# Kernel tuning notes

Measured on AMD Instinct MI355X. Metric: run time of the kernel, lower is better.

The kernel has to match this reference:

```python
import jax, jax.numpy as jnp
import numpy as np

N_NODES = 50000


def _gcn_conv(x, row, col, W, b, n_nodes):
    # symmetric-norm GCN conv with self loops already appended to (row, col)
    deg = jax.ops.segment_sum(jnp.ones_like(row, dtype=x.dtype), row, num_segments=n_nodes)
    # every node has a self loop, so deg >= 1; pow(-0.5) is finite
    dis = deg ** -0.5
    norm = dis[row] * dis[col]                       # [E']
    msg = x[row] * norm[:, None]                     # gather + scale  [E', d]
    agg = jax.ops.segment_sum(msg, col, num_segments=n_nodes)  # scatter-add [N, d]
    return agg @ W + b


def setup_inputs() -> dict:
    key = jax.random.key(0)
    ks = jax.random.split(key, 12)
    N, E, Q, d_in, h = N_NODES, 800000, 200000, 64, 128
    x = jax.random.normal(ks[0], (N, d_in), dtype=jnp.float32)
    edge_index = jax.random.randint(ks[1], (2, E), 0, N)
    edge_label_index = jax.random.randint(ks[2], (2, Q), 0, N)
    def lin(k, fan_in, fan_out):
        kw, kb = jax.random.split(k)
        bound = 1.0 / np.sqrt(fan_in)
        W = jax.random.uniform(kw, (fan_in, fan_out), minval=-bound, maxval=bound, dtype=jnp.float32)
        b = jax.random.uniform(kb, (fan_out,), minval=-bound, maxval=bound, dtype=jnp.float32)
        return W, b
    W1, b1 = lin(ks[3], d_in, h)
    W2, b2 = lin(ks[4], h, h)
    Wc1, bc1 = lin(ks[5], 2 * h, h)
    Wc2, bc2 = lin(ks[6], h, 1)
    return {"x": x, "edge_index": edge_index, "edge_label_index": edge_label_index,
            "W1": W1, "b1": b1, "W2": W2, "b2": b2,
            "Wc1": Wc1, "bc1": bc1, "Wc2": Wc2, "bc2": bc2}


def reference(x, edge_index, edge_label_index, W1, b1, W2, b2, Wc1, bc1, Wc2, bc2):
    n = x.shape[0]
    loops = jnp.arange(n, dtype=edge_index.dtype)
    row = jnp.concatenate([edge_index[0], loops])
    col = jnp.concatenate([edge_index[1], loops])
    h1 = jax.nn.relu(_gcn_conv(x, row, col, W1, b1, n))
    h2 = _gcn_conv(h1, row, col, W2, b2, n)
    src, dst = edge_label_index[0], edge_label_index[1]
    h = jnp.concatenate([h2[src], h2[dst]], axis=1)  # [Q, 2*hidden]
    h = jax.nn.relu(h @ Wc1 + bc1)
    return h @ Wc2 + bc2                              # [Q, 1]
```

## Files before the change

kernel.cpp:

```cpp
#include <hip/hip_runtime.h>


#define HB 64
#define NWIN 16384

typedef __attribute__((ext_vector_type(8))) short short8;
typedef __attribute__((ext_vector_type(4))) float floatx4;

static __device__ __forceinline__ unsigned int f2bf(float v) {
    union { float f; unsigned int u; } c; c.f = v;
    unsigned int lsb = (c.u >> 16) & 1u;
    c.u += 0x7FFFu + lsb;
    return c.u >> 16;
}
static __device__ __forceinline__ float bf2f(unsigned int h) {
    union { float f; unsigned int u; } c; c.u = h << 16;
    return c.f;
}

__global__ __launch_bounds__(256) void k_pre(const int* __restrict__ row,
                                             const int* __restrict__ col,
                                             unsigned int* __restrict__ hRow,
                                             unsigned int* __restrict__ hCol,
                                             const float* __restrict__ x,
                                             unsigned int* __restrict__ xb,
                                             const float* __restrict__ W1,
                                             const float* __restrict__ W2,
                                             const float* __restrict__ Wc1,
                                             const float* __restrict__ b2,
                                             const float* __restrict__ bc1,
                                             unsigned short* __restrict__ UVhi,
                                             unsigned short* __restrict__ UVlo,
                                             unsigned short* __restrict__ W1hi,
                                             unsigned short* __restrict__ W1lo,
                                             float* __restrict__ buv,
                                             int E, int N, int W, int chunk,
                                             int nHist, int nXb) {
    __shared__ unsigned int lds[NWIN];
    int t = threadIdx.x, b = blockIdx.x;
    if (b < nHist) {
        int hb = b % HB;
        int yb = b / HB;
        int p = yb >> 1, win = yb & 1;
        int base = win * NWIN;
        int wcap = min(W - base, NWIN);
        if (wcap <= 0) return;
        const int* idxArr = p ? col : row;
        unsigned int* outArr = p ? hCol : hRow;
        int e0 = hb * chunk, e1 = min(E, e0 + chunk);
        for (int i = t; i < wcap; i += 256) lds[i] = 0;
        __syncthreads();
        for (int e = e0 + t; e < e1; e += 256) {
            int idx = idxArr[e];
            int w = (idx >> 1) - base;
            if ((unsigned)w < (unsigned)wcap)
                atomicAdd(&lds[w], 1u << ((idx & 1) * 16));
        }
        __syncthreads();
        for (int i = t; i < wcap; i += 256)
            outArr[(size_t)hb * W + base + i] = lds[i];
    } else if (b < nHist + nXb) {
        int i = (b - nHist) * 256 + t;
        if (i < N * 32) {
            float2 v = ((const float2*)x)[i];
            xb[i] = f2bf(v.x) | (f2bf(v.y) << 16);
        }
    } else {
        int bf = b - nHist - nXb;
        float* w2row = (float*)lds;
        if (bf < 128) {
            int k = bf;
            int j = t & 127, half = t >> 7;
            int n = half * 128 + j;
            const float* wc = Wc1 + (size_t)half * 128 * 128 + j;
            if (t < 128) w2row[t] = W2[k * 128 + t];
            __syncthreads();
            float acc = 0.f;
#pragma unroll 8
            for (int m = 0; m < 128; m++) acc += w2row[m] * wc[(size_t)m * 128];
            int kstep = k >> 5, kl = k & 31, quad = kl >> 3, j8 = kl & 7;
            int nb = n >> 4, l = quad * 16 + (n & 15);
            int pidx = ((kstep * 16 + nb) * 64 + l) * 8 + j8;
            unsigned int h = f2bf(acc);
            UVhi[pidx] = (unsigned short)h;
            UVlo[pidx] = (unsigned short)f2bf(acc - bf2f(h));
        } else if (bf == 128) {
            int j = t & 127, half = t >> 7;
            const float* wc = Wc1 + (size_t)half * 128 * 128 + j;
            float acc = half ? 0.f : bc1[j];
#pragma unroll 8
            for (int m = 0; m < 128; m++) acc += b2[m] * wc[(size_t)m * 128];
            buv[half * 128 + j] = acc;
        } else {
            int idx = (bf - 129) * 256 + t;
            int k = idx >> 7, n = idx & 127;
            float v = W1[k * 128 + n];
            int kstep = k >> 5, kl = k & 31, quad = kl >> 3, j8 = kl & 7;
            int nb = n >> 4, l = quad * 16 + (n & 15);
            int pidx = ((kstep * 8 + nb) * 64 + l) * 8 + j8;
            unsigned int h = f2bf(v);
            W1hi[pidx] = (unsigned short)h;
            W1lo[pidx] = (unsigned short)f2bf(v - bf2f(h));
        }
    }
}

__global__ __launch_bounds__(256) void k_rs(const unsigned int* __restrict__ hRow,
                                            unsigned int* __restrict__ hCol,
                                            float* __restrict__ dis,
                                            int* __restrict__ offs,
                                            int* __restrict__ bsum,
                                            int N, int W) {
    __shared__ int ts[256];
    int t = threadIdx.x;
    int w = blockIdx.x * 256 + t;
    unsigned int r0 = 0, r1 = 0, c0 = 0, c1 = 0;
    if (w < W) {
#pragma unroll 8
        for (int b = 0; b < HB; b++) {
            size_t idx = (size_t)b * W + w;
            unsigned int hr = hRow[idx];
            unsigned int hc = hCol[idx];
            hCol[idx] = c0 | (c1 << 16);
            r0 += hr & 0xFFFFu; r1 += hr >> 16;
            c0 += hc & 0xFFFFu; c1 += hc >> 16;
        }
        int n0 = 2 * w, n1 = 2 * w + 1;
        dis[n0] = 1.0f / sqrtf((float)(r0 + 1));
        if (n1 < N) dis[n1] = 1.0f / sqrtf((float)(r1 + 1));
    }
    int sum = (w < W) ? (int)(c0 + c1) : 0;
    ts[t] = sum;
    __syncthreads();
    for (int off = 1; off < 256; off <<= 1) {
        int xv = (t >= off) ? ts[t - off] : 0;
        __syncthreads();
        ts[t] += xv;
        __syncthreads();
    }
    int e = ts[t] - sum;
    if (w < W) {
        int n0 = 2 * w, n1 = 2 * w + 1;
        offs[n0] = e;
        if (n1 < N) offs[n1] = e + (int)c0;
    }
    if (t == 255) bsum[blockIdx.x] = ts[255];
}

__global__ __launch_bounds__(256) void k_scan2(int* __restrict__ bsum, int B) {
    __shared__ int ts[256];
    int t = threadIdx.x;
    int v = (t < B) ? bsum[t] : 0;
    ts[t] = v;
    __syncthreads();
    for (int off = 1; off < 256; off <<= 1) {
        int x = (t >= off) ? ts[t - off] : 0;
        __syncthreads();
        ts[t] += x;
        __syncthreads();
    }
    if (t < B) bsum[t] = ts[t] - v;
}

__global__ __launch_bounds__(256) void k_scan3(int* __restrict__ offs,
                                               const int* __restrict__ bsum,
                                               int N, int E) {
    int i = blockIdx.x * 256 + threadIdx.x;
    if (i < N) offs[i] = offs[i] + bsum[i >> 9];
    if (i == 0) offs[N] = E;
}

__global__ __launch_bounds__(256) void k_fill3(const int* __restrict__ row,
                                               const int* __restrict__ col,
                                               const int* __restrict__ offs,
                                               const unsigned int* __restrict__ hCol,
                                               int* __restrict__ srcSorted,
                                               int E, int N, int W, int chunk) {
    __shared__ int base[NWIN];
    int t = threadIdx.x, b = blockIdx.x;
    int n0 = blockIdx.y * NWIN;
    int nCnt = min(NWIN, N - n0);
    int e0 = b * chunk, e1 = min(E, e0 + chunk);
    for (int wl = t; wl * 2 < nCnt; wl += 256) {
        unsigned int pref = hCol[(size_t)b * W + (n0 >> 1) + wl];
        int nn = n0 + wl * 2;
        base[wl * 2] = offs[nn] + (int)(pref & 0xFFFFu);
        if (wl * 2 + 1 < nCnt)
            base[wl * 2 + 1] = offs[nn + 1] + (int)(pref >> 16);
    }
    __syncthreads();
    for (int e = e0 + t; e < e1; e += 256) {
        int c = col[e] - n0;
        if ((unsigned)c < (unsigned)nCnt) {
            int pos = atomicAdd(&base[c], 1);
            srcSorted[pos] = row[e];
        }
    }
}

__global__ __launch_bounds__(256) void k_conv1(const unsigned short* __restrict__ s,
                                               const int* __restrict__ offs,
                                               const int* __restrict__ srcs,
                                               const float* __restrict__ dis,
                                               const unsigned short* __restrict__ Bhi,
                                               const unsigned short* __restrict__ Blo,
                                               const float* __restrict__ b1,
                                               unsigned short* __restrict__ h1b, int N) {
    __shared__ unsigned short Ahi[16][72];
    __shared__ unsigned short Alo[16][72];
    int t = threadIdx.x;
    int lane = t & 63, wave = t >> 6;
    int quad = lane >> 4;
    short8 bh[2][2], bl[2][2];
#pragma unroll
    for (int ks = 0; ks < 2; ks++)
#pragma unroll
        for (int nt = 0; nt < 2; nt++) {
            int nb = wave * 2 + nt;
            bh[ks][nt] = *(const short8*)(Bhi + ((ks * 8 + nb) * 64 + lane) * 8);
            bl[ks][nt] = *(const short8*)(Blo + ((ks * 8 + nb) * 64 + lane) * 8);
        }
    {
        int nl = t >> 4;
        int node = blockIdx.x * 16 + nl;
        if (node < N) {
            int c4 = (t & 15) * 4;
            int e = offs[node], eEnd = offs[node + 1];
            float dn = dis[node];
            uint2 w = *(const uint2*)(s + (size_t)node * 64 + c4);
            float4 acc;
            acc.x = bf2f(w.x & 0xFFFF) * dn; acc.y = bf2f(w.x >> 16) * dn;
            acc.z = bf2f(w.y & 0xFFFF) * dn; acc.w = bf2f(w.y >> 16) * dn;
            while (e + 3 < eEnd) {
                int sA = srcs[e], sB = srcs[e + 1], sC = srcs[e + 2], sD = srcs[e + 3];
                float dA = dis[sA], dB = dis[sB], dC = dis[sC], dD = dis[sD];
                uint2 vA = *(const uint2*)(s + (size_t)sA * 64 + c4);
                uint2 vB = *(const uint2*)(s + (size_t)sB * 64 + c4);
                uint2 vC = *(const uint2*)(s + (size_t)sC * 64 + c4);
                uint2 vD = *(const uint2*)(s + (size_t)sD * 64 + c4);
                acc.x += bf2f(vA.x & 0xFFFF) * dA + bf2f(vB.x & 0xFFFF) * dB;
                acc.y += bf2f(vA.x >> 16) * dA + bf2f(vB.x >> 16) * dB;
                acc.z += bf2f(vA.y & 0xFFFF) * dA + bf2f(vB.y & 0xFFFF) * dB;
                acc.w += bf2f(vA.y >> 16) * dA + bf2f(vB.y >> 16) * dB;
                acc.x += bf2f(vC.x & 0xFFFF) * dC + bf2f(vD.x & 0xFFFF) * dD;
                acc.y += bf2f(vC.x >> 16) * dC + bf2f(vD.x >> 16) * dD;
                acc.z += bf2f(vC.y & 0xFFFF) * dC + bf2f(vD.y & 0xFFFF) * dD;
                acc.w += bf2f(vC.y >> 16) * dC + bf2f(vD.y >> 16) * dD;
                e += 4;
            }
            while (e + 1 < eEnd) {
                int sA = srcs[e], sB = srcs[e + 1];
                float dA = dis[sA], dB = dis[sB];
                uint2 vA = *(const uint2*)(s + (size_t)sA * 64 + c4);
                uint2 vB = *(const uint2*)(s + (size_t)sB * 64 + c4);
                acc.x += bf2f(vA.x & 0xFFFF) * dA + bf2f(vB.x & 0xFFFF) * dB;
                acc.y += bf2f(vA.x >> 16) * dA + bf2f(vB.x >> 16) * dB;
                acc.z += bf2f(vA.y & 0xFFFF) * dA + bf2f(vB.y & 0xFFFF) * dB;
                acc.w += bf2f(vA.y >> 16) * dA + bf2f(vB.y >> 16) * dB;
                e += 2;
            }
            if (e < eEnd) {
                int sA = srcs[e];
                float dA = dis[sA];
                uint2 vA = *(const uint2*)(s + (size_t)sA * 64 + c4);
                acc.x += bf2f(vA.x & 0xFFFF) * dA; acc.y += bf2f(vA.x >> 16) * dA;
                acc.z += bf2f(vA.y & 0xFFFF) * dA; acc.w += bf2f(vA.y >> 16) * dA;
            }
            acc.x *= dn; acc.y *= dn; acc.z *= dn; acc.w *= dn;
            unsigned int h0 = f2bf(acc.x), h1 = f2bf(acc.y),
                         h2 = f2bf(acc.z), h3 = f2bf(acc.w);
            uint2 hw; hw.x = h0 | (h1 << 16); hw.y = h2 | (h3 << 16);
            uint2 lw;
            lw.x = f2bf(acc.x - bf2f(h0)) | (f2bf(acc.y - bf2f(h1)) << 16);
            lw.y = f2bf(acc.z - bf2f(h2)) | (f2bf(acc.w - bf2f(h3)) << 16);
            *(uint2*)(&Ahi[nl][c4]) = hw;
            *(uint2*)(&Alo[nl][c4]) = lw;
        }
    }
    __syncthreads();
    int ml = lane & 15;
    floatx4 acc[2] = {};
#pragma unroll
    for (int ks = 0; ks < 2; ks++) {
        short8 ahi = *(const short8*)(&Ahi[ml][ks * 32 + quad * 8]);
        short8 alo = *(const short8*)(&Alo[ml][ks * 32 + quad * 8]);
#pragma unroll
        for (int nt = 0; nt < 2; nt++) {
            acc[nt] = __builtin_amdgcn_mfma_f32_16x16x32_bf16(ahi, bh[ks][nt], acc[nt], 0, 0, 0);
            acc[nt] = __builtin_amdgcn_mfma_f32_16x16x32_bf16(ahi, bl[ks][nt], acc[nt], 0, 0, 0);
            acc[nt] = __builtin_amdgcn_mfma_f32_16x16x32_bf16(alo, bh[ks][nt], acc[nt], 0, 0, 0);
        }
    }
    int md = blockIdx.x * 16 + quad * 4;
#pragma unroll
    for (int nt = 0; nt < 2; nt++) {
        int n0 = (wave * 2 + nt) * 16 + (lane & 15);
        float bias = b1[n0];
#pragma unroll
        for (int r = 0; r < 4; r++) {
            int node = md + r;
            if (node < N)
                h1b[(size_t)node * 128 + n0] =
                    (unsigned short)f2bf(fmaxf(acc[nt][r] + bias, 0.f) * dis[node]);
        }
    }
}

__global__ __launch_bounds__(512) void k_conv2(const unsigned short* __restrict__ s,
                                               const int* __restrict__ offs,
                                               const int* __restrict__ srcs,
                                               const float* __restrict__ dis,
                                               const unsigned short* __restrict__ Bhi,
                                               const unsigned short* __restrict__ Blo,
                                               const float* __restrict__ buv,
                                               unsigned short* __restrict__ Ub,
                                               unsigned short* __restrict__ Vb, int N) {
    __shared__ unsigned short Ab[32][136];
    int t = threadIdx.x;
    {
        int nl = t >> 4;
        int node = blockIdx.x * 32 + nl;
        int c8 = (t & 15) * 8;
        if (node < N) {
            int e = offs[node], eEnd = offs[node + 1];
            float dn = dis[node];
            uint4 w = *(const uint4*)(s + (size_t)node * 128 + c8);
            float a0 = bf2f(w.x & 0xFFFF), a1 = bf2f(w.x >> 16);
            float a2 = bf2f(w.y & 0xFFFF), a3 = bf2f(w.y >> 16);
            float a4 = bf2f(w.z & 0xFFFF), a5 = bf2f(w.z >> 16);
            float a6 = bf2f(w.w & 0xFFFF), a7 = bf2f(w.w >> 16);
            while (e + 7 < eEnd) {
                int s0 = srcs[e],     s1 = srcs[e + 1], s2 = srcs[e + 2], s3 = srcs[e + 3];
                int s4 = srcs[e + 4], s5 = srcs[e + 5], s6 = srcs[e + 6], s7 = srcs[e + 7];
                uint4 v0 = *(const uint4*)(s + (size_t)s0 * 128 + c8);
                uint4 v1 = *(const uint4*)(s + (size_t)s1 * 128 + c8);
                uint4 v2 = *(const uint4*)(s + (size_t)s2 * 128 + c8);
                uint4 v3 = *(const uint4*)(s + (size_t)s3 * 128 + c8);
                uint4 v4 = *(const uint4*)(s + (size_t)s4 * 128 + c8);
                uint4 v5 = *(const uint4*)(s + (size_t)s5 * 128 + c8);
                uint4 v6 = *(const uint4*)(s + (size_t)s6 * 128 + c8);
                uint4 v7 = *(const uint4*)(s + (size_t)s7 * 128 + c8);
                a0 += bf2f(v0.x & 0xFFFF) + bf2f(v1.x & 0xFFFF);
                a1 += bf2f(v0.x >> 16) + bf2f(v1.x >> 16);
                a2 += bf2f(v0.y & 0xFFFF) + bf2f(v1.y & 0xFFFF);
                a3 += bf2f(v0.y >> 16) + bf2f(v1.y >> 16);
                a4 += bf2f(v0.z & 0xFFFF) + bf2f(v1.z & 0xFFFF);
                a5 += bf2f(v0.z >> 16) + bf2f(v1.z >> 16);
                a6 += bf2f(v0.w & 0xFFFF) + bf2f(v1.w & 0xFFFF);
                a7 += bf2f(v0.w >> 16) + bf2f(v1.w >> 16);
                a0 += bf2f(v2.x & 0xFFFF) + bf2f(v3.x & 0xFFFF);
                a1 += bf2f(v2.x >> 16) + bf2f(v3.x >> 16);
                a2 += bf2f(v2.y & 0xFFFF) + bf2f(v3.y & 0xFFFF);
                a3 += bf2f(v2.y >> 16) + bf2f(v3.y >> 16);
                a4 += bf2f(v2.z & 0xFFFF) + bf2f(v3.z & 0xFFFF);
                a5 += bf2f(v2.z >> 16) + bf2f(v3.z >> 16);
                a6 += bf2f(v2.w & 0xFFFF) + bf2f(v3.w & 0xFFFF);
                a7 += bf2f(v2.w >> 16) + bf2f(v3.w >> 16);
                a0 += bf2f(v4.x & 0xFFFF) + bf2f(v5.x & 0xFFFF);
                a1 += bf2f(v4.x >> 16) + bf2f(v5.x >> 16);
                a2 += bf2f(v4.y & 0xFFFF) + bf2f(v5.y & 0xFFFF);
                a3 += bf2f(v4.y >> 16) + bf2f(v5.y >> 16);
                a4 += bf2f(v4.z & 0xFFFF) + bf2f(v5.z & 0xFFFF);
                a5 += bf2f(v4.z >> 16) + bf2f(v5.z >> 16);
                a6 += bf2f(v4.w & 0xFFFF) + bf2f(v5.w & 0xFFFF);
                a7 += bf2f(v4.w >> 16) + bf2f(v5.w >> 16);
                a0 += bf2f(v6.x & 0xFFFF) + bf2f(v7.x & 0xFFFF);
                a1 += bf2f(v6.x >> 16) + bf2f(v7.x >> 16);
                a2 += bf2f(v6.y & 0xFFFF) + bf2f(v7.y & 0xFFFF);
                a3 += bf2f(v6.y >> 16) + bf2f(v7.y >> 16);
                a4 += bf2f(v6.z & 0xFFFF) + bf2f(v7.z & 0xFFFF);
                a5 += bf2f(v6.z >> 16) + bf2f(v7.z >> 16);
                a6 += bf2f(v6.w & 0xFFFF) + bf2f(v7.w & 0xFFFF);
                a7 += bf2f(v6.w >> 16) + bf2f(v7.w >> 16);
                e += 8;
            }
            while (e + 3 < eEnd) {
                int sA = srcs[e], sB = srcs[e + 1], sC = srcs[e + 2], sD = srcs[e + 3];
                uint4 vA = *(const uint4*)(s + (size_t)sA * 128 + c8);
                uint4 vB = *(const uint4*)(s + (size_t)sB * 128 + c8);
                uint4 vC = *(const uint4*)(s + (size_t)sC * 128 + c8);
                uint4 vD = *(const uint4*)(s + (size_t)sD * 128 + c8);
                a0 += bf2f(vA.x & 0xFFFF) + bf2f(vB.x & 0xFFFF);
                a1 += bf2f(vA.x >> 16) + bf2f(vB.x >> 16);
                a2 += bf2f(vA.y & 0xFFFF) + bf2f(vB.y & 0xFFFF);
                a3 += bf2f(vA.y >> 16) + bf2f(vB.y >> 16);
                a4 += bf2f(vA.z & 0xFFFF) + bf2f(vB.z & 0xFFFF);
                a5 += bf2f(vA.z >> 16) + bf2f(vB.z >> 16);
                a6 += bf2f(vA.w & 0xFFFF) + bf2f(vB.w & 0xFFFF);
                a7 += bf2f(vA.w >> 16) + bf2f(vB.w >> 16);
                a0 += bf2f(vC.x & 0xFFFF) + bf2f(vD.x & 0xFFFF);
                a1 += bf2f(vC.x >> 16) + bf2f(vD.x >> 16);
                a2 += bf2f(vC.y & 0xFFFF) + bf2f(vD.y & 0xFFFF);
                a3 += bf2f(vC.y >> 16) + bf2f(vD.y >> 16);
                a4 += bf2f(vC.z & 0xFFFF) + bf2f(vD.z & 0xFFFF);
                a5 += bf2f(vC.z >> 16) + bf2f(vD.z >> 16);
                a6 += bf2f(vC.w & 0xFFFF) + bf2f(vD.w & 0xFFFF);
                a7 += bf2f(vC.w >> 16) + bf2f(vD.w >> 16);
                e += 4;
            }
            while (e + 1 < eEnd) {
                int sA = srcs[e], sB = srcs[e + 1];
                uint4 vA = *(const uint4*)(s + (size_t)sA * 128 + c8);
                uint4 vB = *(const uint4*)(s + (size_t)sB * 128 + c8);
                a0 += bf2f(vA.x & 0xFFFF) + bf2f(vB.x & 0xFFFF);
                a1 += bf2f(vA.x >> 16) + bf2f(vB.x >> 16);
                a2 += bf2f(vA.y & 0xFFFF) + bf2f(vB.y & 0xFFFF);
                a3 += bf2f(vA.y >> 16) + bf2f(vB.y >> 16);
                a4 += bf2f(vA.z & 0xFFFF) + bf2f(vB.z & 0xFFFF);
                a5 += bf2f(vA.z >> 16) + bf2f(vB.z >> 16);
                a6 += bf2f(vA.w & 0xFFFF) + bf2f(vB.w & 0xFFFF);
                a7 += bf2f(vA.w >> 16) + bf2f(vB.w >> 16);
                e += 2;
            }
            if (e < eEnd) {
                int sA = srcs[e];
                uint4 vA = *(const uint4*)(s + (size_t)sA * 128 + c8);
                a0 += bf2f(vA.x & 0xFFFF); a1 += bf2f(vA.x >> 16);
                a2 += bf2f(vA.y & 0xFFFF); a3 += bf2f(vA.y >> 16);
                a4 += bf2f(vA.z & 0xFFFF); a5 += bf2f(vA.z >> 16);
                a6 += bf2f(vA.w & 0xFFFF); a7 += bf2f(vA.w >> 16);
            }
            uint4 o;
            o.x = f2bf(a0 * dn) | (f2bf(a1 * dn) << 16);
            o.y = f2bf(a2 * dn) | (f2bf(a3 * dn) << 16);
            o.z = f2bf(a4 * dn) | (f2bf(a5 * dn) << 16);
            o.w = f2bf(a6 * dn) | (f2bf(a7 * dn) << 16);
            *(uint4*)(&Ab[nl][c8]) = o;
        } else {
            uint4 z; z.x = 0; z.y = 0; z.z = 0; z.w = 0;
            *(uint4*)(&Ab[nl][c8]) = z;
        }
    }
    int lane = t & 63, wave = t >> 6, quad = lane >> 4, ml = lane & 15;
    short8 bh[4][2], bl[4][2];
#pragma unroll
    for (int ks = 0; ks < 4; ks++)
#pragma unroll
        for (int nt = 0; nt < 2; nt++) {
            int nb = wave * 2 + nt;
            bh[ks][nt] = *(const short8*)(Bhi + ((ks * 16 + nb) * 64 + lane) * 8);
            bl[ks][nt] = *(const short8*)(Blo + ((ks * 16 + nb) * 64 + lane) * 8);
        }
    __syncthreads();
#pragma unroll
    for (int g = 0; g < 2; g++) {
        int mbase = blockIdx.x * 32 + g * 16;
        floatx4 acc[2] = {};
#pragma unroll
        for (int ks = 0; ks < 4; ks++) {
            short8 a = *(const short8*)(&Ab[g * 16 + ml][ks * 32 + quad * 8]);
#pragma unroll
            for (int nt = 0; nt < 2; nt++) {
                acc[nt] = __builtin_amdgcn_mfma_f32_16x16x32_bf16(a, bh[ks][nt], acc[nt], 0, 0, 0);
                acc[nt] = __builtin_amdgcn_mfma_f32_16x16x32_bf16(a, bl[ks][nt], acc[nt], 0, 0, 0);
            }
        }
        int md = mbase + quad * 4;
#pragma unroll
        for (int nt = 0; nt < 2; nt++) {
            int n0 = (wave * 2 + nt) * 16 + ml;
            float bias = buv[n0];
            unsigned short* dst = (n0 < 128) ? Ub : Vb;
            int cc = n0 & 127;
#pragma unroll
            for (int r = 0; r < 4; r++) {
                int nd = md + r;
                if (nd < N)
                    dst[(size_t)nd * 128 + cc] =
                        (unsigned short)f2bf(acc[nt][r] + bias);
            }
        }
    }
}

__global__ __launch_bounds__(256) void k_head(const unsigned short* __restrict__ Ub,
                                              const unsigned short* __restrict__ Vb,
                                              const int* __restrict__ srcA,
                                              const int* __restrict__ dstA,
                                              const float* __restrict__ Wc2,
                                              const float* __restrict__ bc2,
                                              float* __restrict__ out, int Q) {
    int t = threadIdx.x;
    int q = blockIdx.x * 16 + (t >> 4);
    if (q >= Q) return;
    int l = t & 15;
    int s = srcA[q], d = dstA[q];
    uint4 u = *(const uint4*)(Ub + (size_t)s * 128 + l * 8);
    uint4 v = *(const uint4*)(Vb + (size_t)d * 128 + l * 8);
    const float4* w = (const float4*)(Wc2 + l * 8);
    float4 w0 = w[0], w1 = w[1];
    float acc = 0.f, z;
    z = fmaxf(bf2f(u.x & 0xFFFF) + bf2f(v.x & 0xFFFF), 0.f); acc += z * w0.x;
    z = fmaxf(bf2f(u.x >> 16)    + bf2f(v.x >> 16),    0.f); acc += z * w0.y;
    z = fmaxf(bf2f(u.y & 0xFFFF) + bf2f(v.y & 0xFFFF), 0.f); acc += z * w0.z;
    z = fmaxf(bf2f(u.y >> 16)    + bf2f(v.y >> 16),    0.f); acc += z * w0.w;
    z = fmaxf(bf2f(u.z & 0xFFFF) + bf2f(v.z & 0xFFFF), 0.f); acc += z * w1.x;
    z = fmaxf(bf2f(u.z >> 16)    + bf2f(v.z >> 16),    0.f); acc += z * w1.y;
    z = fmaxf(bf2f(u.w & 0xFFFF) + bf2f(v.w & 0xFFFF), 0.f); acc += z * w1.z;
    z = fmaxf(bf2f(u.w >> 16)    + bf2f(v.w >> 16),    0.f); acc += z * w1.w;
    acc += __shfl_xor(acc, 1);
    acc += __shfl_xor(acc, 2);
    acc += __shfl_xor(acc, 4);
    acc += __shfl_xor(acc, 8);
    if (l == 0) out[q] = acc + bc2[0];
}

extern "C" void kernel_launch(void* const* d_in, const int* in_sizes, int n_in,
                              void* d_out, int out_size, void* d_ws, size_t ws_size,
                              hipStream_t stream) {
    const float* x   = (const float*)d_in[0];
    const int*   ei  = (const int*)d_in[1];
    const int*   eli = (const int*)d_in[2];
    const float* W1  = (const float*)d_in[3];
    const float* b1  = (const float*)d_in[4];
    const float* W2  = (const float*)d_in[5];
    const float* b2  = (const float*)d_in[6];
    const float* Wc1 = (const float*)d_in[7];
    const float* bc1 = (const float*)d_in[8];
    const float* Wc2 = (const float*)d_in[9];
    const float* bc2 = (const float*)d_in[10];
    float* out = (float*)d_out;
    char* wsb = (char*)d_ws;

    const int N = in_sizes[0] / 64;
    const int E = in_sizes[1] / 2;
    const int Q = in_sizes[2] / 2;
    const int W = (N + 1) / 2;
    const int chunk = (E + HB - 1) / HB;
    const int nPass = (N + NWIN - 1) / NWIN;
    const int nWinH = (W + NWIN - 1) / NWIN;
    const int nHist = HB * 2 * nWinH;
    const int nXb   = (N * 32 + 255) / 256;
    const int rsB   = (W + 255) / 256;

    float* dis       = (float*)wsb;
    int*   offs      = (int*)wsb + 65536;
    int*   bsum      = (int*)wsb + 197120;
    float* buv       = (float*)wsb + 262912;
    unsigned short* UVhi = (unsigned short*)((int*)wsb + 263168);
    unsigned short* UVlo = (unsigned short*)((int*)wsb + 279552);
    unsigned short* W1hi = (unsigned short*)((int*)wsb + 295936);
    unsigned short* W1lo = (unsigned short*)((int*)wsb + 300032);
    int*   srcSorted = (int*)wsb + 304128;
    unsigned short* Vb   = (unsigned short*)((int*)wsb + 1104128);
    unsigned short* h1b  = (unsigned short*)((int*)wsb + 4304128);
    unsigned short* Ub   = (unsigned short*)((int*)wsb + 7504128);
    unsigned int* hRow = (unsigned int*)wsb + 10704128;
    unsigned int* hCol = (unsigned int*)wsb + 12304128;
    unsigned int* xb   = (unsigned int*)wsb + 13904128;

    const int* row  = ei;
    const int* col  = ei + E;
    const int* srcA = eli;
    const int* dstA = eli + Q;

    k_pre<<<nHist + nXb + 161, 256, 0, stream>>>(
        row, col, hRow, hCol, x, xb, W1, W2, Wc1, b2, bc1,
        UVhi, UVlo, W1hi, W1lo, buv, E, N, W, chunk, nHist, nXb);
    k_rs<<<rsB, 256, 0, stream>>>(hRow, hCol, dis, offs, bsum, N, W);
    k_scan2<<<1, 256, 0, stream>>>(bsum, rsB);
    k_scan3<<<(N + 255) / 256, 256, 0, stream>>>(offs, bsum, N, E);
    k_fill3<<<dim3(HB, nPass), 256, 0, stream>>>(row, col, offs, hCol, srcSorted, E, N, W, chunk);
    k_conv1<<<(N + 15) / 16, 256, 0, stream>>>(
        (const unsigned short*)xb, offs, srcSorted, dis, W1hi, W1lo, b1, h1b, N);
    k_conv2<<<(N + 31) / 32, 512, 0, stream>>>(
        h1b, offs, srcSorted, dis, UVhi, UVlo, buv, Ub, Vb, N);
    k_head<<<(Q + 15) / 16, 256, 0, stream>>>(Ub, Vb, srcA, dstA, Wc2, bc2, out, Q);
}
```

Baseline: 248.3 us.

## Process nodes in in-degree-sorted order in conv kernels for load balance

Builds a counting-sort permutation of nodes by in-degree (capped at 63) from the existing histogram pass, using a global degree histogram, a prefix scan, and atomic placement. The two aggregation kernels then walk nodes through this permutation, so the nodes handled by one block and wavefront have similar edge counts and less lane divergence in the gather loops. In exchange, output writes and node reads become scattered through perm, several atomics are added, and the order within each degree bucket is nondeterministic.

```diff
diff --git a/kernel.cpp b/kernel.cpp
--- a/kernel.cpp
+++ b/kernel.cpp
@@ -34,6 +34,7 @@
                                              unsigned short* __restrict__ W1hi,
                                              unsigned short* __restrict__ W1lo,
                                              float* __restrict__ buv,
+                                             int* __restrict__ dhist,
                                              int E, int N, int W, int chunk,
                                              int nHist, int nXb) {
     __shared__ unsigned int lds[NWIN];
@@ -91,7 +92,7 @@
 #pragma unroll 8
             for (int m = 0; m < 128; m++) acc += b2[m] * wc[(size_t)m * 128];
             buv[half * 128 + j] = acc;
-        } else {
+        } else if (bf < 161) {
             int idx = (bf - 129) * 256 + t;
             int k = idx >> 7, n = idx & 127;
             float v = W1[k * 128 + n];
@@ -101,6 +102,8 @@
             unsigned int h = f2bf(v);
             W1hi[pidx] = (unsigned short)h;
             W1lo[pidx] = (unsigned short)f2bf(v - bf2f(h));
+        } else {
+            if (t < 64) dhist[t] = 0;
         }
     }
 }
@@ -110,6 +113,8 @@
                                             float* __restrict__ dis,
                                             int* __restrict__ offs,
                                             int* __restrict__ bsum,
+                                            int* __restrict__ degA,
+                                            int* __restrict__ dhist,
                                             int N, int W) {
     __shared__ int ts[256];
     int t = threadIdx.x;
@@ -127,7 +132,13 @@
         }
         int n0 = 2 * w, n1 = 2 * w + 1;
         dis[n0] = 1.0f / sqrtf((float)(r0 + 1));
-        if (n1 < N) dis[n1] = 1.0f / sqrtf((float)(r1 + 1));
+        degA[n0] = (int)c0;
+        atomicAdd(&dhist[min((int)c0, 63)], 1);
+        if (n1 < N) {
+            dis[n1] = 1.0f / sqrtf((float)(r1 + 1));
+            degA[n1] = (int)c1;
+            atomicAdd(&dhist[min((int)c1, 63)], 1);
+        }
     }
     int sum = (w < W) ? (int)(c0 + c1) : 0;
     ts[t] = sum;
@@ -147,7 +158,8 @@
     if (t == 255) bsum[blockIdx.x] = ts[255];
 }
 
-__global__ __launch_bounds__(256) void k_scan2(int* __restrict__ bsum, int B) {
+__global__ __launch_bounds__(256) void k_scan2(int* __restrict__ bsum,
+                                               int* __restrict__ dhist, int B) {
     __shared__ int ts[256];
     int t = threadIdx.x;
     int v = (t < B) ? bsum[t] : 0;
@@ -160,13 +172,31 @@
         __syncthreads();
     }
     if (t < B) bsum[t] = ts[t] - v;
+    __syncthreads();
+    int hv = (t < 64) ? dhist[t] : 0;
+    ts[t] = hv;
+    __syncthreads();
+    for (int off = 1; off < 64; off <<= 1) {
+        int x = (t >= off && t < 64) ? ts[t - off] : 0;
+        __syncthreads();
+        if (t < 64) ts[t] += x;
+        __syncthreads();
+    }
+    if (t < 64) dhist[t] = ts[t] - hv;
 }
 
 __global__ __launch_bounds__(256) void k_scan3(int* __restrict__ offs,
                                                const int* __restrict__ bsum,
+                                               const int* __restrict__ degA,
+                                               int* __restrict__ dhist,
+                                               int* __restrict__ perm,
                                                int N, int E) {
     int i = blockIdx.x * 256 + threadIdx.x;
-    if (i < N) offs[i] = offs[i] + bsum[i >> 9];
+    if (i < N) {
+        offs[i] = offs[i] + bsum[i >> 9];
+        int pos = atomicAdd(&dhist[min(degA[i], 63)], 1);
+        perm[pos] = i;
+    }
     if (i == 0) offs[N] = E;
 }
 
@@ -202,6 +232,7 @@
                                                const int* __restrict__ offs,
                                                const int* __restrict__ srcs,
                                                const float* __restrict__ dis,
+                                               const int* __restrict__ perm,
                                                const unsigned short* __restrict__ Bhi,
                                                const unsigned short* __restrict__ Blo,
                                                const float* __restrict__ b1,
@@ -222,8 +253,9 @@
         }
     {
         int nl = t >> 4;
-        int node = blockIdx.x * 16 + nl;
-        if (node < N) {
+        int oi = blockIdx.x * 16 + nl;
+        if (oi < N) {
+            int node = perm[oi];
             int c4 = (t & 15) * 4;
             int e = offs[node], eEnd = offs[node + 1];
             float dn = dis[node];
@@ -298,10 +330,12 @@
         float bias = b1[n0];
 #pragma unroll
         for (int r = 0; r < 4; r++) {
-            int node = md + r;
-            if (node < N)
+            int oi = md + r;
+            if (oi < N) {
+                int node = perm[oi];
                 h1b[(size_t)node * 128 + n0] =
                     (unsigned short)f2bf(fmaxf(acc[nt][r] + bias, 0.f) * dis[node]);
+            }
         }
     }
 }
@@ -310,6 +344,7 @@
                                                const int* __restrict__ offs,
                                                const int* __restrict__ srcs,
                                                const float* __restrict__ dis,
+                                               const int* __restrict__ perm,
                                                const unsigned short* __restrict__ Bhi,
                                                const unsigned short* __restrict__ Blo,
                                                const float* __restrict__ buv,
@@ -319,9 +354,10 @@
     int t = threadIdx.x;
     {
         int nl = t >> 4;
-        int node = blockIdx.x * 32 + nl;
+        int oi = blockIdx.x * 32 + nl;
         int c8 = (t & 15) * 8;
-        if (node < N) {
+        if (oi < N) {
+            int node = perm[oi];
             int e = offs[node], eEnd = offs[node + 1];
             float dn = dis[node];
             uint4 w = *(const uint4*)(s + (size_t)node * 128 + c8);
@@ -464,10 +500,12 @@
             int cc = n0 & 127;
 #pragma unroll
             for (int r = 0; r < 4; r++) {
-                int nd = md + r;
-                if (nd < N)
-                    dst[(size_t)nd * 128 + cc] =
+                int oi = md + r;
+                if (oi < N) {
+                    int node = perm[oi];
+                    dst[(size_t)node * 128 + cc] =
                         (unsigned short)f2bf(acc[nt][r] + bias);
+                }
             }
         }
     }
@@ -535,7 +573,10 @@
 
     float* dis       = (float*)wsb;
     int*   offs      = (int*)wsb + 65536;
+    int*   degA      = (int*)wsb + 115584;
+    int*   dhist     = (int*)wsb + 165584;
     int*   bsum      = (int*)wsb + 197120;
+    int*   perm      = (int*)wsb + 197632;
     float* buv       = (float*)wsb + 262912;
     unsigned short* UVhi = (unsigned short*)((int*)wsb + 263168);
     unsigned short* UVlo = (unsigned short*)((int*)wsb + 279552);
@@ -554,16 +595,16 @@
     const int* srcA = eli;
     const int* dstA = eli + Q;
 
-    k_pre<<<nHist + nXb + 161, 256, 0, stream>>>(
+    k_pre<<<nHist + nXb + 162, 256, 0, stream>>>(
         row, col, hRow, hCol, x, xb, W1, W2, Wc1, b2, bc1,
-        UVhi, UVlo, W1hi, W1lo, buv, E, N, W, chunk, nHist, nXb);
-    k_rs<<<rsB, 256, 0, stream>>>(hRow, hCol, dis, offs, bsum, N, W);
-    k_scan2<<<1, 256, 0, stream>>>(bsum, rsB);
-    k_scan3<<<(N + 255) / 256, 256, 0, stream>>>(offs, bsum, N, E);
+        UVhi, UVlo, W1hi, W1lo, buv, dhist, E, N, W, chunk, nHist, nXb);
+    k_rs<<<rsB, 256, 0, stream>>>(hRow, hCol, dis, offs, bsum, degA, dhist, N, W);
+    k_scan2<<<1, 256, 0, stream>>>(bsum, dhist, rsB);
+    k_scan3<<<(N + 255) / 256, 256, 0, stream>>>(offs, bsum, degA, dhist, perm, N, E);
     k_fill3<<<dim3(HB, nPass), 256, 0, stream>>>(row, col, offs, hCol, srcSorted, E, N, W, chunk);
     k_conv1<<<(N + 15) / 16, 256, 0, stream>>>(
-        (const unsigned short*)xb, offs, srcSorted, dis, W1hi, W1lo, b1, h1b, N);
+        (const unsigned short*)xb, offs, srcSorted, dis, perm, W1hi, W1lo, b1, h1b, N);
     k_conv2<<<(N + 31) / 32, 512, 0, stream>>>(
-        h1b, offs, srcSorted, dis, UVhi, UVlo, buv, Ub, Vb, N);
+        h1b, offs, srcSorted, dis, perm, UVhi, UVlo, buv, Ub, Vb, N);
     k_head<<<(Q + 15) / 16, 256, 0, stream>>>(Ub, Vb, srcA, dstA, Wc2, bc2, out, Q);
 }
```

Result: slower. 460.1 us (+85.3%).
